# Optimization experiments

Measured on AMD Instinct MI355X. Metric: run time of the kernel, lower is better.

The kernel has to match this reference:

```python
import jax, jax.numpy as jnp
import numpy as np
import math

D_MODEL = 1024
D_HEAD = 64
N_HEADS = D_MODEL // D_HEAD  # 16
COND = 768
EPS = 1e-6


def make_freqs():
    # AxialRoPE(dim=d_head//2, n_heads): freqs linspace in log-space, reshaped [dim//4, nh].T
    dim = D_HEAD // 2  # 32
    n = N_HEADS * dim // 4  # 128
    log_min = math.log(math.pi)
    log_max = math.log(10.0 * math.pi)
    freqs = jnp.exp(jnp.linspace(log_min, log_max, n + 1, dtype=jnp.float32)[:-1])
    return freqs.reshape(dim // 4, N_HEADS).T  # [n_heads, d_head//8] = [16, 8]


def setup_inputs() -> dict:
    key = jax.random.key(0)
    ks = jax.random.split(key, 6)
    N, H, W = 8, 32, 32
    x = jax.random.normal(ks[0], (N, H, W, D_MODEL), jnp.float32)
    pos = jax.random.uniform(ks[1], (N, H, W, 2), jnp.float32) * 2.0 - 1.0
    cond = jax.random.normal(ks[2], (N, COND), jnp.float32)
    norm_w = jax.random.normal(ks[3], (D_MODEL, COND), jnp.float32) * 0.02
    qkv_w = jax.random.normal(ks[4], (3 * D_MODEL, D_MODEL), jnp.float32) / math.sqrt(D_MODEL)
    out_w = jax.random.normal(ks[5], (D_MODEL, D_MODEL), jnp.float32) * 0.02
    scale = jnp.full((N_HEADS,), 10.0, jnp.float32)
    return {"x": x, "pos": pos, "cond": cond, "norm_w": norm_w,
            "qkv_w": qkv_w, "out_w": out_w, "scale": scale}


def rms_norm(x, scale, eps):
    mean_sq = jnp.mean(x * x, axis=-1, keepdims=True)
    return x * (scale * jax.lax.rsqrt(mean_sq + eps))


def apply_rotary(x, theta):
    # rotate first 2*d dims of the head; rest passes through
    d = theta.shape[-1]
    x1, x2, rest = x[..., :d], x[..., d:2 * d], x[..., 2 * d:]
    cos, sin = jnp.cos(theta), jnp.sin(theta)
    return jnp.concatenate([x1 * cos - x2 * sin, x2 * cos + x1 * sin, rest], axis=-1)


def reference(x, pos, cond, norm_w, qkv_w, out_w, scale):
    N, H, W, _ = x.shape
    S = H * W
    skip = x
    # AdaRMSNorm: scale = zero-init linear(cond) + 1
    ns = cond @ norm_w.T  # [N, d_model]
    xn = rms_norm(x, ns[:, None, None, :] + 1.0, EPS)
    # QKV projection, split 'n h w (t nh e)'
    qkv = (xn @ qkv_w.T).reshape(N, S, 3, N_HEADS, D_HEAD)
    q = jnp.transpose(qkv[:, :, 0], (0, 2, 1, 3))  # [N, nh, S, e]
    k = jnp.transpose(qkv[:, :, 1], (0, 2, 1, 3))
    v = jnp.transpose(qkv[:, :, 2], (0, 2, 1, 3))
    # cosine-sim scaling: per-head learned scale, L2-normalize q,k
    sqrt_scale = jnp.sqrt(scale)[:, None, None]  # [nh,1,1]
    q = q * (sqrt_scale * jax.lax.rsqrt(jnp.sum(q * q, -1, keepdims=True) + EPS))
    k = k * (sqrt_scale * jax.lax.rsqrt(jnp.sum(k * k, -1, keepdims=True) + EPS))
    # axial RoPE theta
    freqs = make_freqs()  # [nh, d_head//8]
    pos_f = pos.reshape(N, S, 2)
    theta_h = pos_f[:, :, None, 0:1] * freqs  # [N,S,nh,8]
    theta_w = pos_f[:, :, None, 1:2] * freqs
    theta = jnp.concatenate([theta_h, theta_w], axis=-1)  # [N,S,nh,16]
    theta = jnp.transpose(theta, (0, 2, 1, 3))  # [N,nh,S,16]
    q = apply_rotary(q, theta)
    k = apply_rotary(k, theta)
    # attention with scale=1.0 (cosine-sim already scaled)
    scores = jnp.einsum('bhqe,bhke->bhqk', q, k)
    probs = jax.nn.softmax(scores, axis=-1)
    o = jnp.einsum('bhqk,bhke->bhqe', probs, v)  # [N,nh,S,e]
    o = jnp.transpose(o, (0, 2, 1, 3)).reshape(N, H, W, D_MODEL)
    return o @ out_w.T + skip
```

## Files before the change

kernel.cpp:

```cpp
#include <hip/hip_runtime.h>
#include <hip/hip_bf16.h>
#include <math.h>

typedef __bf16 bf16;
typedef __bf16 bf16x8 __attribute__((ext_vector_type(8)));
typedef __bf16 bf16x4 __attribute__((ext_vector_type(4)));
typedef float f32x4 __attribute__((ext_vector_type(4)));
typedef float f32x16 __attribute__((ext_vector_type(16)));

#define MFMA16(a, b, c) __builtin_amdgcn_mfma_f32_16x16x32_bf16((a), (b), (c), 0, 0, 0)
#define MFMA32(a, b, c) __builtin_amdgcn_mfma_f32_32x32x16_bf16((a), (b), (c), 0, 0, 0)

__device__ __forceinline__ void gload_lds16(const void* g, void* l) {
  __builtin_amdgcn_global_load_lds((__attribute__((address_space(1))) void*)(g),
                                   (__attribute__((address_space(3))) void*)(l),
                                   16, 0, 0);
}

__global__ __launch_bounds__(256) void f2bf_kernel(const float* __restrict__ in,
                                                   bf16* __restrict__ out, int n4) {
  int i = blockIdx.x * 256 + threadIdx.x;
  if (i >= n4) return;
  float4 v = ((const float4*)in)[i];
  bf16x4 o;
  o[0] = (bf16)v.x; o[1] = (bf16)v.y; o[2] = (bf16)v.z; o[3] = (bf16)v.w;
  *(bf16x4*)(out + (size_t)i * 4) = o;
}

__global__ __launch_bounds__(256) void ns_kernel(const float* __restrict__ cond,
                                                 const float* __restrict__ norm_w,
                                                 float* __restrict__ nsp1) {
  int tid = blockIdx.x * 256 + threadIdx.x;
  int b = tid >> 10, c = tid & 1023;
  const float4* wv = (const float4*)(norm_w + (size_t)c * 768);
  const float4* cv = (const float4*)(cond + (size_t)b * 768);
  float acc = 0.f;
#pragma unroll 8
  for (int i = 0; i < 192; ++i) {
    float4 w4 = wv[i], c4 = cv[i];
    acc += w4.x * c4.x + w4.y * c4.y + w4.z * c4.z + w4.w * c4.w;
  }
  nsp1[tid] = acc + 1.0f;
}

__global__ __launch_bounds__(256) void rmsnorm_kernel(const float* __restrict__ x,
                                                      const float* __restrict__ nsp1,
                                                      bf16* __restrict__ xn) {
  int lane = threadIdx.x & 63, w = threadIdx.x >> 6;
  int m = blockIdx.x * 4 + w;
  int b = m >> 10;
  const float* xp = x + (size_t)m * 1024 + lane * 16;
  float v[16];
  float ss = 0.f;
#pragma unroll
  for (int i = 0; i < 4; ++i) {
    float4 t4 = ((const float4*)xp)[i];
    v[4 * i + 0] = t4.x; v[4 * i + 1] = t4.y; v[4 * i + 2] = t4.z; v[4 * i + 3] = t4.w;
    ss += t4.x * t4.x + t4.y * t4.y + t4.z * t4.z + t4.w * t4.w;
  }
#pragma unroll
  for (int off = 32; off >= 1; off >>= 1) ss += __shfl_xor(ss, off);
  float r = rsqrtf(ss * (1.0f / 1024.0f) + 1e-6f);
  const float* np = nsp1 + (size_t)b * 1024 + lane * 16;
  bf16x8 o0, o1;
#pragma unroll
  for (int j = 0; j < 8; ++j) o0[j] = (bf16)(v[j] * np[j] * r);
#pragma unroll
  for (int j = 0; j < 8; ++j) o1[j] = (bf16)(v[8 + j] * np[8 + j] * r);
  bf16* op = xn + (size_t)m * 1024 + lane * 16;
  *(bf16x8*)op = o0;
  *(bf16x8*)(op + 8) = o1;
}

template <int MODE>
__global__ __launch_bounds__(512, 2) void gemm256b(const bf16* __restrict__ A,
                                                   const bf16* __restrict__ B, int nbn,
                                                   bf16* __restrict__ qout, bf16* __restrict__ kout,
                                                   bf16* __restrict__ vtout, float* __restrict__ fout,
                                                   const float* __restrict__ skip,
                                                   const float* __restrict__ pos,
                                                   const float* __restrict__ scale) {
  constexpr int K = 1024;
  __shared__ __align__(16) bf16 sm[24576];
  const int t = threadIdx.x;
  const int cpx = gridDim.x >> 3;
  const int bid = blockIdx.x;
  const int virt = (bid & 7) * cpx + (bid >> 3);
  const int bn = virt % nbn, bm = virt / nbn;
  const int m0 = bm * 256, n0 = bn * 128;
  const int lane = t & 63, wid = t >> 6;
  const int wr = wid >> 1, wc = wid & 1;
  const int r16 = lane & 15, hi = lane >> 4;

  const int tq = t >> 3, c8 = t & 7, cp = c8 ^ (tq & 7);
  const size_t gA = (size_t)(m0 + tq * 2 + (cp >> 2)) * K + (cp & 3) * 8;
  const size_t gB = (size_t)(n0 + tq * 2 + (cp >> 2)) * K + (cp & 3) * 8;
  const size_t gj = (size_t)128 * K;
  const int ldst = t * 8;

  const int chunk = ((r16 & 1) * 4 + hi) ^ (r16 >> 1);
  int aoff[4], boff[4];
#pragma unroll
  for (int fr = 0; fr < 4; ++fr) aoff[fr] = (wr * 32 + fr * 8 + (r16 >> 1)) * 64 + chunk * 8;
#pragma unroll
  for (int fc = 0; fc < 4; ++fc)
    boff[fc] = (wc * 32 + fc * 8 + (r16 >> 1)) * 64 + chunk * 8 + 8192;

  f32x4 acc[4][4] = {};
  constexpr int NS = K >> 5;

#define STG(tile, slot)                                              \
  {                                                                  \
    const bf16* as_ = A + gA + (size_t)(tile) * 32;                  \
    const bf16* bs_ = B + gB + (size_t)(tile) * 32;                  \
    gload_lds16(as_, &sm[(slot) * 12288 + ldst]);                    \
    gload_lds16(as_ + gj, &sm[(slot) * 12288 + 4096 + ldst]);        \
    gload_lds16(bs_, &sm[(slot) * 12288 + 8192 + ldst]);             \
  }

  STG(0, 0);
  STG(1, 1);

  for (int s = 0; s < NS; ++s) {
    if (s < NS - 1) {
      asm volatile("s_waitcnt vmcnt(3)" ::: "memory");
    } else {
      asm volatile("s_waitcnt vmcnt(0)" ::: "memory");
    }
    __builtin_amdgcn_s_barrier();
    __builtin_amdgcn_sched_barrier(0);
    bf16x8 af[4], bfr[4];
    const bf16* base = &sm[(s & 1) * 12288];
#pragma unroll
    for (int fr = 0; fr < 4; ++fr) af[fr] = *(const bf16x8*)&base[aoff[fr]];
#pragma unroll
    for (int fc = 0; fc < 4; ++fc) bfr[fc] = *(const bf16x8*)&base[boff[fc]];
    asm volatile("s_waitcnt lgkmcnt(0)" ::: "memory");
    __builtin_amdgcn_sched_barrier(0);
    __builtin_amdgcn_s_barrier();
    __builtin_amdgcn_sched_barrier(0);
    if (s + 2 < NS) STG(s + 2, s & 1);
    __builtin_amdgcn_s_setprio(1);
#pragma unroll
    for (int fc = 0; fc < 4; ++fc)
#pragma unroll
      for (int fr = 0; fr < 4; ++fr) acc[fr][fc] = MFMA16(af[fr], bfr[fc], acc[fr][fc]);
    __builtin_amdgcn_s_setprio(0);
  }
#undef STG

  if constexpr (MODE == 0) {
    const int p = n0 >> 10;
    if (p == 2) {
      const int hiq = ((hi & 1) << 1) | (hi >> 1);
#pragma unroll
      for (int fr = 0; fr < 4; ++fr) {
        int mrow = m0 + wr * 64 + fr * 16 + hiq * 4;
        int b = mrow >> 10, s0 = mrow & 1023;
#pragma unroll
        for (int fc = 0; fc < 4; ++fc) {
          int n = n0 + wc * 64 + fc * 16 + r16;
          int d = n & 63, hh = (n >> 6) & 15;
          bf16x4 pk;
          pk[0] = (bf16)acc[fr][fc][0]; pk[1] = (bf16)acc[fr][fc][1];
          pk[2] = (bf16)acc[fr][fc][2]; pk[3] = (bf16)acc[fr][fc][3];
          *(bf16x4*)&vtout[(((size_t)(b * 16 + hh) * 64 + d) << 10) + s0] = pk;
        }
      }
    } else {
      const int hh = ((n0 + wc * 64) >> 6) & 15;
      const float LOG2E = 1.4426950408889634f;
      const float sqv = sqrtf(scale[hh]) * (p == 0 ? LOG2E : 1.0f);
      const float f = __expf(1.14472988584940017f +
                             0.0179897502011134460f * (float)((r16 & 7) * 16 + hh));
      const bool is_h = (r16 < 8);
      bf16* dst = (p == 0) ? qout : kout;
#pragma unroll
      for (int fr = 0; fr < 4; ++fr) {
        int mrow = m0 + wr * 64 + fr * 16 + hi * 4;
        int b = mrow >> 10, s0 = mrow & 1023;
        float rr[4];
#pragma unroll
        for (int r = 0; r < 4; ++r) {
          float ss = acc[fr][0][r] * acc[fr][0][r] + acc[fr][1][r] * acc[fr][1][r] +
                     acc[fr][2][r] * acc[fr][2][r] + acc[fr][3][r] * acc[fr][3][r];
          ss += __shfl_xor(ss, 1);
          ss += __shfl_xor(ss, 2);
          ss += __shfl_xor(ss, 4);
          ss += __shfl_xor(ss, 8);
          rr[r] = sqv * rsqrtf(ss + 1e-6f);
        }
#pragma unroll
        for (int r = 0; r < 4; ++r) {
          float2 pp = *(const float2*)&pos[(((size_t)b << 10) + s0 + r) * 2];
          float th = (is_h ? pp.x : pp.y) * f;
          float sv, cv;
          __sincosf(th, &sv, &cv);
          float x1 = acc[fr][0][r] * rr[r];
          float x2 = acc[fr][1][r] * rr[r];
          size_t rowb = (((size_t)(b * 16 + hh) << 10) + s0 + r) * 64;
          dst[rowb + r16]      = (bf16)(x1 * cv - x2 * sv);
          dst[rowb + 16 + r16] = (bf16)(x2 * cv + x1 * sv);
          dst[rowb + 32 + r16] = (bf16)(acc[fr][2][r] * rr[r]);
          dst[rowb + 48 + r16] = (bf16)(acc[fr][3][r] * rr[r]);
        }
      }
    }
  } else {
#pragma unroll
    for (int fr = 0; fr < 4; ++fr) {
      int mrow = m0 + wr * 64 + fr * 16 + hi * 4;
#pragma unroll
      for (int fc = 0; fc < 4; ++fc) {
        int n = n0 + wc * 64 + fc * 16 + r16;
#pragma unroll
        for (int r = 0; r < 4; ++r) {
          size_t off = (size_t)(mrow + r) * 1024 + n;
          fout[off] = acc[fr][fc][r] + skip[off];
        }
      }
    }
  }
}

__global__ __launch_bounds__(256, 4) void attn_kernel(const bf16* __restrict__ q,
                                                      const bf16* __restrict__ k,
                                                      const bf16* __restrict__ vt,
                                                      bf16* __restrict__ o) {
  int bid = blockIdx.x;
  int virt = (bid & 7) * 128 + (bid >> 3);
  const int bh = virt >> 3;
  const int qt = virt & 7;
  const int b = bh >> 4, h = bh & 15;
  const int t = threadIdx.x, lane = t & 63, w = t >> 6;
  const int l31 = lane & 31, h2 = lane >> 5;

  __shared__ bf16 lK[2][4096];
  __shared__ bf16 lV[2][4096];

  const bf16* kp = k + (size_t)bh * 65536;
  const bf16* vp = vt + (size_t)bh * 65536;

  const bf16* qp = q + ((size_t)bh * 1024 + qt * 128 + w * 32) * 64;
  bf16x8 qf[4];
#pragma unroll
  for (int df = 0; df < 4; ++df)
    qf[df] = *(const bf16x8*)&qp[l31 * 64 + df * 16 + h2 * 8];

  bf16x8 ones;
#pragma unroll
  for (int i = 0; i < 8; ++i) ones[i] = (bf16)1.0f;

  const int srow0 = t >> 3, sc0 = t & 7;

  f32x16 oacc0 = {}, oacc1 = {}, lacc = {};

#pragma unroll
  for (int j = 0; j < 2; ++j) {
    int row = srow0 + j * 32;
    int se = ((sc0 ^ (row & 7)) << 3);
    gload_lds16(kp + (size_t)row * 64 + se, &lK[0][t * 8 + j * 2048]);
    gload_lds16(vp + (size_t)row * 1024 + se, &lV[0][t * 8 + j * 2048]);
  }
  __syncthreads();

  int cur = 0;
  for (int kt = 0; kt < 16; ++kt) {
    if (kt < 15) {
      const bf16* kt_base = kp + (kt + 1) * 4096;
      const bf16* vt_base = vp + (kt + 1) * 64;
#pragma unroll
      for (int j = 0; j < 2; ++j) {
        int row = srow0 + j * 32;
        int se = ((sc0 ^ (row & 7)) << 3);
        gload_lds16(kt_base + (size_t)row * 64 + se, &lK[cur ^ 1][t * 8 + j * 2048]);
        gload_lds16(vt_base + (size_t)row * 1024 + se, &lV[cur ^ 1][t * 8 + j * 2048]);
      }
    }
    f32x16 sa0 = {}, sa1 = {};
    __builtin_amdgcn_s_setprio(1);
#pragma unroll
    for (int df = 0; df < 4; ++df) {
      int sw = l31 & 7;
      int ce = (((2 * df + h2) ^ sw) << 3);
      bf16x8 kf0 = *(const bf16x8*)&lK[cur][l31 * 64 + ce];
      bf16x8 kf1 = *(const bf16x8*)&lK[cur][(32 + l31) * 64 + ce];
      sa0 = MFMA32(kf0, qf[df], sa0);
      sa1 = MFMA32(kf1, qf[df], sa1);
    }
    __builtin_amdgcn_s_setprio(0);
    bf16x8 pa[4];
#pragma unroll
    for (int e = 0; e < 8; ++e) {
      pa[0][e] = (bf16)exp2f(sa0[e]);
      pa[1][e] = (bf16)exp2f(sa0[e + 8]);
      pa[2][e] = (bf16)exp2f(sa1[e]);
      pa[3][e] = (bf16)exp2f(sa1[e + 8]);
    }
    __builtin_amdgcn_s_setprio(1);
#pragma unroll
    for (int pk = 0; pk < 4; ++pk) {
      lacc = MFMA32(pa[pk], ones, lacc);
#pragma unroll
      for (int db = 0; db < 2; ++db) {
        int row = db * 32 + l31, sw = row & 7;
        bf16x8 vf = *(const bf16x8*)&lV[cur][row * 64 + (((2 * pk + h2) ^ sw) << 3)];
        if (db == 0) oacc0 = MFMA32(pa[pk], vf, oacc0);
        else         oacc1 = MFMA32(pa[pk], vf, oacc1);
      }
    }
    __builtin_amdgcn_s_setprio(0);
    __syncthreads();
    cur ^= 1;
  }
  f32x16 inv;
#pragma unroll
  for (int r = 0; r < 16; ++r) inv[r] = 1.f / lacc[r];
#pragma unroll
  for (int r = 0; r < 16; ++r) {
    int qrow = qt * 128 + w * 32 + (r & 3) + 8 * (r >> 2) + 4 * h2;
    size_t rowb = ((size_t)b * 1024 + qrow) * 1024 + h * 64;
    o[rowb + l31]      = (bf16)(oacc0[r] * inv[r]);
    o[rowb + 32 + l31] = (bf16)(oacc1[r] * inv[r]);
  }
}

extern "C" void kernel_launch(void* const* d_in, const int* in_sizes, int n_in,
                              void* d_out, int out_size, void* d_ws, size_t ws_size,
                              hipStream_t stream) {
  const float* x      = (const float*)d_in[0];
  const float* pos    = (const float*)d_in[1];
  const float* cond   = (const float*)d_in[2];
  const float* norm_w = (const float*)d_in[3];
  const float* qkv_w  = (const float*)d_in[4];
  const float* out_w  = (const float*)d_in[5];
  const float* scale  = (const float*)d_in[6];
  float* out = (float*)d_out;

  char* ws = (char*)d_ws;
  bf16* xn        = (bf16*)(ws + 0);
  bf16* qkv_w_bf  = (bf16*)(ws + 16777216);
  bf16* out_w_bf  = (bf16*)(ws + 23068672);
  float* nsp1     = (float*)(ws + 25165824);
  bf16* qraw      = (bf16*)(ws + 25198592);
  bf16* kraw      = (bf16*)(ws + 41975808);
  bf16* vt        = (bf16*)(ws + 58753024);
  bf16* o_attn    = xn;

  f2bf_kernel<<<3072, 256, 0, stream>>>(qkv_w, qkv_w_bf, 786432);
  f2bf_kernel<<<1024, 256, 0, stream>>>(out_w, out_w_bf, 262144);
  ns_kernel<<<32, 256, 0, stream>>>(cond, norm_w, nsp1);
  rmsnorm_kernel<<<2048, 256, 0, stream>>>(x, nsp1, xn);
  gemm256b<0><<<768, 512, 0, stream>>>(xn, qkv_w_bf, 24, qraw, kraw, vt, nullptr, nullptr,
                                       pos, scale);
  attn_kernel<<<1024, 256, 0, stream>>>(qraw, kraw, vt, o_attn);
  gemm256b<1><<<256, 512, 0, stream>>>(o_attn, out_w_bf, 8, nullptr, nullptr, nullptr, out, x,
                                       nullptr, nullptr);
}
```

Baseline: 192.5 us.

## Restructure attention K/V prefetch with vmcnt waits, merge weight casts, raise occupancy

The attention loop now issues K/V tile loads two iterations ahead. It replaces __syncthreads with explicit vmcnt waits and raw barriers, so global-to-LDS loads overlap more with MFMA work. The launch bound is raised to 5 waves per SIMD to allow more resident blocks, which may cause register spills. The two fp32-to-bf16 weight conversion launches are merged into one kernel to cut launch overhead.

```diff
diff --git a/kernel.cpp b/kernel.cpp
--- a/kernel.cpp
+++ b/kernel.cpp
@@ -17,14 +17,18 @@
                                    16, 0, 0);
 }
 
-__global__ __launch_bounds__(256) void f2bf_kernel(const float* __restrict__ in,
-                                                   bf16* __restrict__ out, int n4) {
+__global__ __launch_bounds__(256) void f2bf_kernel(const float* __restrict__ in0,
+                                                   bf16* __restrict__ out0,
+                                                   const float* __restrict__ in1,
+                                                   bf16* __restrict__ out1, int n0) {
   int i = blockIdx.x * 256 + threadIdx.x;
-  if (i >= n4) return;
-  float4 v = ((const float4*)in)[i];
+  const float* in = (i < n0) ? in0 : in1;
+  bf16* out = (i < n0) ? out0 : out1;
+  int j = (i < n0) ? i : i - n0;
+  float4 v = ((const float4*)in)[j];
   bf16x4 o;
   o[0] = (bf16)v.x; o[1] = (bf16)v.y; o[2] = (bf16)v.z; o[3] = (bf16)v.w;
-  *(bf16x4*)(out + (size_t)i * 4) = o;
+  *(bf16x4*)(out + (size_t)j * 4) = o;
 }
 
 __global__ __launch_bounds__(256) void ns_kernel(const float* __restrict__ cond,
@@ -223,7 +227,7 @@
   }
 }
 
-__global__ __launch_bounds__(256, 4) void attn_kernel(const bf16* __restrict__ q,
+__global__ __launch_bounds__(256, 5) void attn_kernel(const bf16* __restrict__ q,
                                                       const bf16* __restrict__ k,
                                                       const bf16* __restrict__ vt,
                                                       bf16* __restrict__ o) {
@@ -255,28 +259,30 @@
 
   f32x16 oacc0 = {}, oacc1 = {}, lacc = {};
 
-#pragma unroll
-  for (int j = 0; j < 2; ++j) {
-    int row = srow0 + j * 32;
-    int se = ((sc0 ^ (row & 7)) << 3);
-    gload_lds16(kp + (size_t)row * 64 + se, &lK[0][t * 8 + j * 2048]);
-    gload_lds16(vp + (size_t)row * 1024 + se, &lV[0][t * 8 + j * 2048]);
-  }
-  __syncthreads();
-
-  int cur = 0;
+#define STGA(kt_, buf_)                                                            \
+  {                                                                                \
+    const bf16* kb_ = kp + (kt_) * 4096;                                           \
+    const bf16* vb_ = vp + (kt_) * 64;                                             \
+    _Pragma("unroll") for (int j = 0; j < 2; ++j) {                                \
+      int row = srow0 + j * 32;                                                    \
+      int se = ((sc0 ^ (row & 7)) << 3);                                           \
+      gload_lds16(kb_ + (size_t)row * 64 + se, &lK[buf_][t * 8 + j * 2048]);       \
+      gload_lds16(vb_ + (size_t)row * 1024 + se, &lV[buf_][t * 8 + j * 2048]);     \
+    }                                                                              \
+  }
+
+  STGA(0, 0);
+  STGA(1, 1);
+
   for (int kt = 0; kt < 16; ++kt) {
+    const int cur = kt & 1;
     if (kt < 15) {
-      const bf16* kt_base = kp + (kt + 1) * 4096;
-      const bf16* vt_base = vp + (kt + 1) * 64;
-#pragma unroll
-      for (int j = 0; j < 2; ++j) {
-        int row = srow0 + j * 32;
-        int se = ((sc0 ^ (row & 7)) << 3);
-        gload_lds16(kt_base + (size_t)row * 64 + se, &lK[cur ^ 1][t * 8 + j * 2048]);
-        gload_lds16(vt_base + (size_t)row * 1024 + se, &lV[cur ^ 1][t * 8 + j * 2048]);
-      }
-    }
+      asm volatile("s_waitcnt vmcnt(4)" ::: "memory");
+    } else {
+      asm volatile("s_waitcnt vmcnt(0)" ::: "memory");
+    }
+    __builtin_amdgcn_s_barrier();
+    __builtin_amdgcn_sched_barrier(0);
     f32x16 sa0 = {}, sa1 = {};
     __builtin_amdgcn_s_setprio(1);
 #pragma unroll
@@ -310,9 +316,13 @@
       }
     }
     __builtin_amdgcn_s_setprio(0);
-    __syncthreads();
-    cur ^= 1;
-  }
+    __builtin_amdgcn_sched_barrier(0);
+    __builtin_amdgcn_s_barrier();
+    __builtin_amdgcn_sched_barrier(0);
+    if (kt < 14) STGA(kt + 2, cur);
+  }
+#undef STGA
+
   f32x16 inv;
 #pragma unroll
   for (int r = 0; r < 16; ++r) inv[r] = 1.f / lacc[r];
@@ -347,8 +357,7 @@
   bf16* vt        = (bf16*)(ws + 58753024);
   bf16* o_attn    = xn;
 
-  f2bf_kernel<<<3072, 256, 0, stream>>>(qkv_w, qkv_w_bf, 786432);
-  f2bf_kernel<<<1024, 256, 0, stream>>>(out_w, out_w_bf, 262144);
+  f2bf_kernel<<<4096, 256, 0, stream>>>(qkv_w, qkv_w_bf, out_w, out_w_bf, 786432);
   ns_kernel<<<32, 256, 0, stream>>>(cond, norm_w, nsp1);
   rmsnorm_kernel<<<2048, 256, 0, stream>>>(x, nsp1, xn);
   gemm256b<0><<<768, 512, 0, stream>>>(xn, qkv_w_bf, 24, qraw, kraw, vt, nullptr, nullptr,
```

New measurement: 284.9 us. 48.0% more time.
